# Optimization experiments

Measured on AMD Instinct MI355X. Metric: run time of the kernel, lower is better.

The kernel has to match this reference:

```python
import jax, jax.numpy as jnp
import numpy as np

N, F = 400000, 128
M = 100000
DENSE = [256, 256, 128]


def setup_inputs() -> dict:
    key = jax.random.key(0)
    ks = jax.random.split(key, 8)
    x = jax.random.normal(ks[0], (N, F), dtype=jnp.float32)
    sel_idx = jax.random.randint(ks[1], (M, 1), 0, N, dtype=jnp.int32)
    # Dense layer params, scaled like glorot-ish init
    W0 = jax.random.normal(ks[2], (F, DENSE[0]), dtype=jnp.float32) * (1.0 / np.sqrt(F))
    b0 = jnp.zeros((DENSE[0],), dtype=jnp.float32)
    W1 = jax.random.normal(ks[3], (DENSE[0], DENSE[1]), dtype=jnp.float32) * (1.0 / np.sqrt(DENSE[0]))
    b1 = jnp.zeros((DENSE[1],), dtype=jnp.float32)
    W2 = jax.random.normal(ks[4], (DENSE[1], DENSE[2]), dtype=jnp.float32) * (1.0 / np.sqrt(DENSE[1]))
    b2 = jnp.zeros((DENSE[2],), dtype=jnp.float32)
    return {"x": x, "sel_idx": sel_idx, "W0": W0, "b0": b0,
            "W1": W1, "b1": b1, "W2": W2, "b2": b2}


def reference(x, sel_idx, W0, b0, W1, b1, W2, b2):
    idx = sel_idx[:, 0]                       # [M]
    up = x[idx]                               # gather_nd -> [M, F]
    up = jax.nn.elu(up @ W0 + b0)             # [M, 256]
    up = jax.nn.elu(up @ W1 + b1)             # [M, 256]
    up = jax.nn.elu(up @ W2 + b2)             # [M, F]
    # x += scatter_nd(sel_idx, up, shape(x))
    return x + jnp.zeros_like(x).at[idx].add(up)
```

## Files before the change

kernel.cpp:

```cpp
#include <hip/hip_runtime.h>
#include <hip/hip_bf16.h>

#define NROWS 400000
#define MSEL  100000
#define FDIM  128
#define D0 256
#define D1 256
#define D2 128

typedef __attribute__((ext_vector_type(8))) short short8;
typedef __attribute__((ext_vector_type(4))) float f32x4;
typedef __attribute__((ext_vector_type(4))) unsigned short ushort4v;

__device__ __forceinline__ unsigned short f2bf(float f) {
    unsigned int u = __float_as_uint(f);
    unsigned int r = (u + 0x7fffu + ((u >> 16) & 1u)) >> 16;
    return (unsigned short)r;
}

__device__ __forceinline__ float elu(float v) {
    return v > 0.f ? v : (__expf(v) - 1.f);
}

__global__ void pack_weights(const float* __restrict__ W0,
                             const float* __restrict__ W1,
                             const float* __restrict__ W2,
                             short* __restrict__ out) {
    int e = blockIdx.x * 256 + threadIdx.x;
    if (e >= 131072) return;
    const float* W; int N; int base; int le;
    if (e < 32768)       { W = W0; N = 256; base = 0;     le = e; }
    else if (e < 98304)  { W = W1; N = 256; base = 32768; le = e - 32768; }
    else                 { W = W2; N = 128; base = 98304; le = e - 98304; }
    int t    = le >> 9;
    int r    = le & 511;
    int lane = r >> 3;
    int j    = r & 7;
    int ntiles = N >> 4;
    int kt = t / ntiles, nt = t % ntiles;
    int k = kt * 32 + (lane >> 4) * 8 + j;
    int n = nt * 16 + (lane & 15);
    out[base + le] = (short)f2bf(W[k * N + n]);
}

__global__ void copy_x(const float4* __restrict__ x, float4* __restrict__ out, int n4) {
    int i = blockIdx.x * blockDim.x + threadIdx.x;
    int stride = gridDim.x * blockDim.x;
    for (; i < n4; i += stride) out[i] = x[i];
}

__global__ void init_head(int* __restrict__ head) {
    int i = blockIdx.x * 256 + threadIdx.x;
    int s = gridDim.x * 256;
    for (; i < NROWS; i += s) head[i] = -1;
}

__global__ void build_links(const int* __restrict__ sel,
                            int* __restrict__ head, int* __restrict__ next) {
    int j = blockIdx.x * 256 + threadIdx.x;
    if (j < MSEL) {
        int r = sel[j];
        next[j] = atomicExch(head + r, j);
    }
}

template <bool SPLIT>
__global__ __launch_bounds__(256) void mlp_compute(
    const float* __restrict__ x, const int* __restrict__ sel,
    const short* __restrict__ wp,
    const float* __restrict__ b0v, const float* __restrict__ b1v,
    const float* __restrict__ b2v,
    unsigned short* __restrict__ upOut, float* __restrict__ out) {
    __shared__ __align__(16) short lds[20480];

    const int tid  = threadIdx.x;
    const int lane = tid & 63;
    const int w    = tid >> 6;
    const int rowBase = blockIdx.x * 32;
    const int lm = lane & 15;
    const int kq = lane >> 4;
    const int sxz = (lm & 7) << 3;

    const short* W0p = wp;
    const short* W1p = wp + 32768;
    const short* W2p = wp + 98304;

    short8 B0[4][4];
    #pragma unroll
    for (int kt = 0; kt < 4; kt++)
        #pragma unroll
        for (int ntl = 0; ntl < 4; ntl++)
            B0[kt][ntl] = *(const short8*)(W0p + ((kt * 16 + (w * 4 + ntl)) * 512 + lane * 8));

    const float4* xv = (const float4*)x;
    #pragma unroll
    for (int it = 0; it < 4; it++) {
        int i = it * 256 + tid;
        int row = i >> 5, seg = i & 31;
        float4 v = xv[(size_t)sel[rowBase + row] * 32 + seg];
        ushort4v p = { f2bf(v.x), f2bf(v.y), f2bf(v.z), f2bf(v.w) };
        *(ushort4v*)(&lds[(row * 128 + seg * 4) ^ ((row & 7) << 3)]) = p;
    }
    __syncthreads();

    const f32x4 zero4 = {0.f, 0.f, 0.f, 0.f};

    {
        f32x4 acc[2][4];
        #pragma unroll
        for (int i = 0; i < 2; i++)
            #pragma unroll
            for (int j = 0; j < 4; j++) acc[i][j] = zero4;
        #pragma unroll
        for (int rt = 0; rt < 2; rt++) {
            short8 a[4];
            int rowA = rt * 16 + lm;
            #pragma unroll
            for (int kt = 0; kt < 4; kt++)
                a[kt] = *(const short8*)(&lds[(rowA * 128 + kt * 32 + kq * 8) ^ sxz]);
            #pragma unroll
            for (int ntl = 0; ntl < 4; ntl++)
                #pragma unroll
                for (int kt = 0; kt < 4; kt++)
                    acc[rt][ntl] = __builtin_amdgcn_mfma_f32_16x16x32_bf16(a[kt], B0[kt][ntl], acc[rt][ntl], 0, 0, 0);
        }
        #pragma unroll
        for (int ntl = 0; ntl < 4; ntl++) {
            int col = (w * 4 + ntl) * 16 + lm;
            float bias = b0v[col];
            #pragma unroll
            for (int rt = 0; rt < 2; rt++)
                #pragma unroll
                for (int r = 0; r < 4; r++) {
                    int row = rt * 16 + kq * 4 + r;
                    float v = elu(acc[rt][ntl][r] + bias);
                    lds[4096 + ((row * 256 + col) ^ ((row & 7) << 3))] = (short)f2bf(v);
                }
        }
    }
    __syncthreads();

    #pragma unroll
    for (int pass = 0; pass < 2; pass++) {
        short8 B1[8][2];
        #pragma unroll
        for (int kt = 0; kt < 8; kt++)
            #pragma unroll
            for (int p = 0; p < 2; p++)
                B1[kt][p] = *(const short8*)(W1p + ((kt * 16 + (w * 4 + pass * 2 + p)) * 512 + lane * 8));
        f32x4 acc[2][2];
        #pragma unroll
        for (int i = 0; i < 2; i++)
            #pragma unroll
            for (int j = 0; j < 2; j++) acc[i][j] = zero4;
        #pragma unroll
        for (int rt = 0; rt < 2; rt++) {
            short8 a[8];
            int rowA = rt * 16 + lm;
            #pragma unroll
            for (int kt = 0; kt < 8; kt++)
                a[kt] = *(const short8*)(&lds[4096 + ((rowA * 256 + kt * 32 + kq * 8) ^ sxz)]);
            #pragma unroll
            for (int p = 0; p < 2; p++)
                #pragma unroll
                for (int kt = 0; kt < 8; kt++)
                    acc[rt][p] = __builtin_amdgcn_mfma_f32_16x16x32_bf16(a[kt], B1[kt][p], acc[rt][p], 0, 0, 0);
        }
        #pragma unroll
        for (int p = 0; p < 2; p++) {
            int col = (w * 4 + pass * 2 + p) * 16 + lm;
            float bias = b1v[col];
            #pragma unroll
            for (int rt = 0; rt < 2; rt++)
                #pragma unroll
                for (int r = 0; r < 4; r++) {
                    int row = rt * 16 + kq * 4 + r;
                    float v = elu(acc[rt][p][r] + bias);
                    lds[12288 + ((row * 256 + col) ^ ((row & 7) << 3))] = (short)f2bf(v);
                }
        }
    }
    __syncthreads();

    {
        short8 B2[8][2];
        #pragma unroll
        for (int kt = 0; kt < 8; kt++)
            #pragma unroll
            for (int ntl = 0; ntl < 2; ntl++)
                B2[kt][ntl] = *(const short8*)(W2p + ((kt * 8 + (w * 2 + ntl)) * 512 + lane * 8));

        f32x4 acc[2][2];
        #pragma unroll
        for (int i = 0; i < 2; i++)
            #pragma unroll
            for (int j = 0; j < 2; j++) acc[i][j] = zero4;
        #pragma unroll
        for (int rt = 0; rt < 2; rt++) {
            short8 a[8];
            int rowA = rt * 16 + lm;
            #pragma unroll
            for (int kt = 0; kt < 8; kt++)
                a[kt] = *(const short8*)(&lds[12288 + ((rowA * 256 + kt * 32 + kq * 8) ^ sxz)]);
            #pragma unroll
            for (int ntl = 0; ntl < 2; ntl++)
                #pragma unroll
                for (int kt = 0; kt < 8; kt++)
                    acc[rt][ntl] = __builtin_amdgcn_mfma_f32_16x16x32_bf16(a[kt], B2[kt][ntl], acc[rt][ntl], 0, 0, 0);
        }
        #pragma unroll
        for (int ntl = 0; ntl < 2; ntl++) {
            int col = (w * 2 + ntl) * 16 + lm;
            float bias = b2v[col];
            #pragma unroll
            for (int rt = 0; rt < 2; rt++)
                #pragma unroll
                for (int r = 0; r < 4; r++) {
                    int row = rt * 16 + kq * 4 + r;
                    int grow = rowBase + row;
                    float v = elu(acc[rt][ntl][r] + bias);
                    if (SPLIT) {
                        upOut[(size_t)grow * 128 + col] = f2bf(v);
                    } else {
                        atomicAdd(out + (size_t)sel[grow] * 128 + col, v);
                    }
                }
        }
    }
}

__global__ __launch_bounds__(256) void merge_out(
    const float2* __restrict__ x2, const unsigned int* __restrict__ up32,
    const int* __restrict__ head, const int* __restrict__ next,
    float2* __restrict__ out2) {
    int wid  = blockIdx.x * 4 + (threadIdx.x >> 6);
    int lane = threadIdx.x & 63;
    int wstride = gridDim.x * 4;
    for (int row = wid; row < NROWS; row += wstride) {
        float2 v = x2[(size_t)row * 64 + lane];
        int j = head[row];
        while (j >= 0) {
            unsigned int u = up32[j * 64 + lane];
            v.x += __uint_as_float(u << 16);
            v.y += __uint_as_float(u & 0xffff0000u);
            j = next[j];
        }
        out2[(size_t)row * 64 + lane] = v;
    }
}

extern "C" void kernel_launch(void* const* d_in, const int* in_sizes, int n_in,
                              void* d_out, int out_size, void* d_ws, size_t ws_size,
                              hipStream_t stream) {
    const float* x   = (const float*)d_in[0];
    const int*   sel = (const int*)d_in[1];
    const float* W0  = (const float*)d_in[2];
    const float* b0  = (const float*)d_in[3];
    const float* W1  = (const float*)d_in[4];
    const float* b1  = (const float*)d_in[5];
    const float* W2  = (const float*)d_in[6];
    const float* b2  = (const float*)d_in[7];
    float* out = (float*)d_out;

    char* wsb = (char*)d_ws;
    short* wp          = (short*)wsb;
    unsigned short* up = (unsigned short*)(wsb + 262144);
    int* head          = (int*)(wsb + 262144 + (size_t)MSEL * 256);
    int* nxt           = head + NROWS;
    const size_t need  = 262144 + (size_t)MSEL * 256 + (size_t)NROWS * 4 + (size_t)MSEL * 4;

    pack_weights<<<512, 256, 0, stream>>>(W0, W1, W2, wp);
    if (ws_size >= need) {
        init_head<<<1024, 256, 0, stream>>>(head);
        build_links<<<(MSEL + 255) / 256, 256, 0, stream>>>(sel, head, nxt);
        mlp_compute<true><<<MSEL / 32, 256, 0, stream>>>(x, sel, wp, b0, b1, b2, up, out);
        merge_out<<<4096, 256, 0, stream>>>((const float2*)x, (const unsigned int*)up,
                                            head, nxt, (float2*)out);
    } else {
        copy_x<<<4096, 256, 0, stream>>>((const float4*)x, (float4*)out, NROWS * FDIM / 4);
        mlp_compute<false><<<MSEL / 32, 256, 0, stream>>>(x, sel, wp, b0, b1, b2, up, out);
    }
}
```

Baseline: 154.2 us.

## Write singly-selected rows directly from MLP kernel and skip them in merge

The MLP kernel now checks, for each selected index, whether it is the only selection of its target row, using the linked list built earlier. For those rows it writes x + up straight to the output instead of staging bf16 up in workspace, and the merge kernel skips them. This removes the up write and read and the second x read for most selected rows. The cost is that x for those rows comes from the bf16 copy in LDS, which loses precision, and there are extra head/next lookups. It also switches the float-to-bf16 conversions to a packed two-value intrinsic.

```diff
diff --git a/kernel.cpp b/kernel.cpp
--- a/kernel.cpp
+++ b/kernel.cpp
@@ -11,11 +11,21 @@
 typedef __attribute__((ext_vector_type(8))) short short8;
 typedef __attribute__((ext_vector_type(4))) float f32x4;
 typedef __attribute__((ext_vector_type(4))) unsigned short ushort4v;
+typedef __attribute__((ext_vector_type(2))) unsigned int uint2v;
 
 __device__ __forceinline__ unsigned short f2bf(float f) {
     unsigned int u = __float_as_uint(f);
     unsigned int r = (u + 0x7fffu + ((u >> 16) & 1u)) >> 16;
     return (unsigned short)r;
+}
+
+__device__ __forceinline__ unsigned int pk2bf(float a, float b) {
+    __hip_bfloat162 h = __float22bfloat162_rn(make_float2(a, b));
+    return *(unsigned int*)&h;
+}
+
+__device__ __forceinline__ float bf2f(unsigned short u) {
+    return __uint_as_float(((unsigned int)u) << 16);
 }
 
 __device__ __forceinline__ float elu(float v) {
@@ -70,6 +80,7 @@
     const short* __restrict__ wp,
     const float* __restrict__ b0v, const float* __restrict__ b1v,
     const float* __restrict__ b2v,
+    const int* __restrict__ head, const int* __restrict__ next,
     unsigned short* __restrict__ upOut, float* __restrict__ out) {
     __shared__ __align__(16) short lds[20480];
 
@@ -98,8 +109,8 @@
         int i = it * 256 + tid;
         int row = i >> 5, seg = i & 31;
         float4 v = xv[(size_t)sel[rowBase + row] * 32 + seg];
-        ushort4v p = { f2bf(v.x), f2bf(v.y), f2bf(v.z), f2bf(v.w) };
-        *(ushort4v*)(&lds[(row * 128 + seg * 4) ^ ((row & 7) << 3)]) = p;
+        uint2v p = { pk2bf(v.x, v.y), pk2bf(v.z, v.w) };
+        *(uint2v*)(&lds[(row * 128 + seg * 4) ^ ((row & 7) << 3)]) = p;
     }
     __syncthreads();
 
@@ -129,13 +140,18 @@
             int col = (w * 4 + ntl) * 16 + lm;
             float bias = b0v[col];
             #pragma unroll
-            for (int rt = 0; rt < 2; rt++)
-                #pragma unroll
-                for (int r = 0; r < 4; r++) {
-                    int row = rt * 16 + kq * 4 + r;
-                    float v = elu(acc[rt][ntl][r] + bias);
-                    lds[4096 + ((row * 256 + col) ^ ((row & 7) << 3))] = (short)f2bf(v);
-                }
+            for (int rt = 0; rt < 2; rt++) {
+                float v0 = elu(acc[rt][ntl][0] + bias);
+                float v1 = elu(acc[rt][ntl][1] + bias);
+                float v2 = elu(acc[rt][ntl][2] + bias);
+                float v3 = elu(acc[rt][ntl][3] + bias);
+                unsigned int u01 = pk2bf(v0, v1), u23 = pk2bf(v2, v3);
+                int row = rt * 16 + kq * 4;
+                lds[4096 + (((row+0) * 256 + col) ^ (((row+0) & 7) << 3))] = (short)(u01 & 0xffff);
+                lds[4096 + (((row+1) * 256 + col) ^ (((row+1) & 7) << 3))] = (short)(u01 >> 16);
+                lds[4096 + (((row+2) * 256 + col) ^ (((row+2) & 7) << 3))] = (short)(u23 & 0xffff);
+                lds[4096 + (((row+3) * 256 + col) ^ (((row+3) & 7) << 3))] = (short)(u23 >> 16);
+            }
         }
     }
     __syncthreads();
@@ -171,13 +187,18 @@
             int col = (w * 4 + pass * 2 + p) * 16 + lm;
             float bias = b1v[col];
             #pragma unroll
-            for (int rt = 0; rt < 2; rt++)
-                #pragma unroll
-                for (int r = 0; r < 4; r++) {
-                    int row = rt * 16 + kq * 4 + r;
-                    float v = elu(acc[rt][p][r] + bias);
-                    lds[12288 + ((row * 256 + col) ^ ((row & 7) << 3))] = (short)f2bf(v);
-                }
+            for (int rt = 0; rt < 2; rt++) {
+                float v0 = elu(acc[rt][p][0] + bias);
+                float v1 = elu(acc[rt][p][1] + bias);
+                float v2 = elu(acc[rt][p][2] + bias);
+                float v3 = elu(acc[rt][p][3] + bias);
+                unsigned int u01 = pk2bf(v0, v1), u23 = pk2bf(v2, v3);
+                int row = rt * 16 + kq * 4;
+                lds[12288 + (((row+0) * 256 + col) ^ (((row+0) & 7) << 3))] = (short)(u01 & 0xffff);
+                lds[12288 + (((row+1) * 256 + col) ^ (((row+1) & 7) << 3))] = (short)(u01 >> 16);
+                lds[12288 + (((row+2) * 256 + col) ^ (((row+2) & 7) << 3))] = (short)(u23 & 0xffff);
+                lds[12288 + (((row+3) * 256 + col) ^ (((row+3) & 7) << 3))] = (short)(u23 >> 16);
+            }
         }
     }
     __syncthreads();
@@ -189,6 +210,19 @@
             #pragma unroll
             for (int ntl = 0; ntl < 2; ntl++)
                 B2[kt][ntl] = *(const short8*)(W2p + ((kt * 8 + (w * 2 + ntl)) * 512 + lane * 8));
+
+        int jj[2][4]; int rr[2][4]; bool sg[2][4];
+        #pragma unroll
+        for (int rt = 0; rt < 2; rt++)
+            #pragma unroll
+            for (int r = 0; r < 4; r++) {
+                int j = rowBase + rt * 16 + kq * 4 + r;
+                jj[rt][r] = j;
+                int t = sel[j];
+                rr[rt][r] = t;
+                if (SPLIT) sg[rt][r] = (next[j] < 0) && (head[t] == j);
+                else       sg[rt][r] = false;
+            }
 
         f32x4 acc[2][2];
         #pragma unroll
@@ -216,13 +250,17 @@
             for (int rt = 0; rt < 2; rt++)
                 #pragma unroll
                 for (int r = 0; r < 4; r++) {
-                    int row = rt * 16 + kq * 4 + r;
-                    int grow = rowBase + row;
+                    int lrow = rt * 16 + kq * 4 + r;
                     float v = elu(acc[rt][ntl][r] + bias);
                     if (SPLIT) {
-                        upOut[(size_t)grow * 128 + col] = f2bf(v);
+                        if (sg[rt][r]) {
+                            float xb = bf2f((unsigned short)lds[(lrow * 128 + col) ^ ((lrow & 7) << 3)]);
+                            out[(size_t)rr[rt][r] * 128 + col] = xb + v;
+                        } else {
+                            upOut[(size_t)jj[rt][r] * 128 + col] = f2bf(v);
+                        }
                     } else {
-                        atomicAdd(out + (size_t)sel[grow] * 128 + col, v);
+                        atomicAdd(out + (size_t)rr[rt][r] * 128 + col, v);
                     }
                 }
         }
@@ -237,15 +275,21 @@
     int lane = threadIdx.x & 63;
     int wstride = gridDim.x * 4;
     for (int row = wid; row < NROWS; row += wstride) {
-        float2 v = x2[(size_t)row * 64 + lane];
         int j = head[row];
-        while (j >= 0) {
-            unsigned int u = up32[j * 64 + lane];
-            v.x += __uint_as_float(u << 16);
-            v.y += __uint_as_float(u & 0xffff0000u);
-            j = next[j];
-        }
-        out2[(size_t)row * 64 + lane] = v;
+        if (j < 0) {
+            out2[(size_t)row * 64 + lane] = x2[(size_t)row * 64 + lane];
+        } else {
+            int nx = next[j];
+            if (nx < 0) continue;
+            float2 v = x2[(size_t)row * 64 + lane];
+            while (j >= 0) {
+                unsigned int u = up32[(size_t)j * 64 + lane];
+                v.x += __uint_as_float(u << 16);
+                v.y += __uint_as_float(u & 0xffff0000u);
+                j = next[j];
+            }
+            out2[(size_t)row * 64 + lane] = v;
+        }
     }
 }
 
@@ -273,11 +317,11 @@
     if (ws_size >= need) {
         init_head<<<1024, 256, 0, stream>>>(head);
         build_links<<<(MSEL + 255) / 256, 256, 0, stream>>>(sel, head, nxt);
-        mlp_compute<true><<<MSEL / 32, 256, 0, stream>>>(x, sel, wp, b0, b1, b2, up, out);
+        mlp_compute<true><<<MSEL / 32, 256, 0, stream>>>(x, sel, wp, b0, b1, b2, head, nxt, up, out);
         merge_out<<<4096, 256, 0, stream>>>((const float2*)x, (const unsigned int*)up,
                                             head, nxt, (float2*)out);
     } else {
         copy_x<<<4096, 256, 0, stream>>>((const float4*)x, (float4*)out, NROWS * FDIM / 4);
-        mlp_compute<false><<<MSEL / 32, 256, 0, stream>>>(x, sel, wp, b0, b1, b2, up, out);
-    }
-}
+        mlp_compute<false><<<MSEL / 32, 256, 0, stream>>>(x, sel, wp, b0, b1, b2, head, nxt, up, out);
+    }
+}
```

Result: slower. 188.7 us (+22.4%).
